# Performance work log

Hardware: AMD Instinct MI355X
Metric: run time of the kernel (lower is better)

## Reference

```python
import jax, jax.numpy as jnp
import numpy as np

N, E = 20000, 320000          # nodes, edges (avg degree 16)
IN, OUT, EC = 256, 256, 64    # in_channels == out_channels (required by BN placement)
BN_EPS = 1e-5


def setup_inputs() -> dict:
    key = jax.random.key(0)
    ks = jax.random.split(key, 8)
    def lin(k, fan_in, fan_out):
        # kaiming-uniform-ish init like nn.Linear
        bound = 1.0 / np.sqrt(fan_in)
        return jax.random.uniform(k, (fan_in, fan_out), jnp.float32, -bound, bound)
    return {
        "x": jax.random.normal(ks[0], (N, IN), jnp.float32),
        "edge_index": jax.random.randint(ks[1], (2, E), 0, N),
        "edge_attr": jax.random.normal(ks[2], (E, EC), jnp.float32),
        "W_edge": lin(ks[3], EC, IN),          # edge_lin (no bias)
        "W_rel": lin(ks[4], IN, OUT),           # GraphConv lin_rel weight
        "b_rel": jnp.zeros((OUT,), jnp.float32),  # GraphConv lin_rel bias
        "W_root": lin(ks[5], IN, OUT),          # GraphConv lin_root (no bias)
        "gamma": jnp.ones((OUT,), jnp.float32),  # BN weight
        "beta": jnp.zeros((OUT,), jnp.float32),  # BN bias
        "W_res": lin(ks[6], IN, OUT),           # res_lin (no bias)
    }


def reference(x, edge_index, edge_attr, W_edge, W_rel, b_rel, W_root, gamma, beta, W_res):
    src, dst = edge_index[0], edge_index[1]
    # edge feature projection: [E, EC] -> [E, IN]
    e = edge_attr @ W_edge
    # message passing: gather source node feats, modulate by edge feats, scatter-add to dst
    msg = x[src] * e                                   # [E, IN]
    agg = jax.ops.segment_sum(msg, dst, num_segments=x.shape[0])  # [N, IN]
    # GraphConv: lin_rel(aggregate) + lin_root(x)
    h = agg @ W_rel + b_rel + x @ W_root               # [N, OUT]
    h = jax.nn.relu(h)
    # BatchNorm1d (training mode: batch statistics over nodes)
    mean = h.mean(axis=0)
    var = ((h - mean) ** 2).mean(axis=0)
    h = (h - mean) * jax.lax.rsqrt(var + BN_EPS) * gamma + beta
    # residual branch
    return h + x @ W_res
```

## Files before the change

### kernel.cpp

```cpp
#include <hip/hip_runtime.h>
#include <hip/hip_bf16.h>


#define N_NODES 20000
#define E_EDGES 320000
#define C 256
#define CE 64
#define MAXDEG 64
#define BN_EPS 1e-5f

typedef __attribute__((ext_vector_type(8))) short short8;
typedef __attribute__((ext_vector_type(8))) unsigned short ushort8;
typedef __attribute__((ext_vector_type(4))) float f32x4;
typedef __attribute__((ext_vector_type(4))) unsigned short ushort4v;

static __device__ __forceinline__ float bf2f(unsigned short u) {
    union { unsigned int i; float f; } v; v.i = (unsigned int)u << 16; return v.f;
}
static __device__ __forceinline__ unsigned short f2bf(float f) {
    __hip_bfloat16 h = __float2bfloat16(f);
    return *reinterpret_cast<unsigned short*>(&h);
}

__global__ __launch_bounds__(256) void k_wprep(
    const float* __restrict__ W_rel, const float* __restrict__ W_root,
    const float* __restrict__ W_res, const float* __restrict__ W_edge,
    unsigned short* __restrict__ wt_hi, unsigned short* __restrict__ wte_hi) {
    int b = blockIdx.x, n = threadIdx.x;
    if (b < 768) {
        int m = b >> 8, k = b & 255;
        const float* W = (m == 0) ? W_rel : (m == 1) ? W_root : W_res;
        size_t o = (((size_t)m * 16 + (n >> 4)) * 8 + (k >> 5)) * 512
                 + (size_t)(((n & 15) | (((k >> 3) & 3) << 4)) * 8) + (k & 7);
        wt_hi[o] = f2bf(W[k * C + n]);
    } else {
        int k = b - 768;
        size_t o = ((size_t)(n >> 4) * 2 + (k >> 5)) * 512
                 + (size_t)(((n & 15) | (((k >> 3) & 3) << 4)) * 8) + (k & 7);
        wte_hi[o] = f2bf(W_edge[k * C + n]);
    }
}

__global__ void k_bucket(const int* __restrict__ ei, int* __restrict__ deg,
                         int2* __restrict__ elist2) {
    int e = blockIdx.x * blockDim.x + threadIdx.x;
    if (e < E_EDGES) {
        int d = ei[E_EDGES + e];
        int s = ei[e];
        int slot = atomicAdd(&deg[d], 1);
        if (slot < MAXDEG) elist2[d * MAXDEG + slot] = make_int2(e, s);
    }
}

__global__ __launch_bounds__(256, 3) void k_edgemm(
    const float* __restrict__ ea, const unsigned short* __restrict__ wte_hi,
    unsigned short* __restrict__ e_mat) {
    __shared__ short lds[16384];
    const int tid = threadIdx.x;
    const int e0 = blockIdx.x * 64;

#pragma unroll
    for (int i = 0; i < 4; ++i) {
        int f = tid + 256 * i;
        int r = f >> 4, k4 = (f & 15) * 4;
        float4 v = *reinterpret_cast<const float4*>(&ea[(size_t)(e0 + r) * CE + k4]);
        unsigned short h0 = f2bf(v.x), h1 = f2bf(v.y), h2 = f2bf(v.z), h3 = f2bf(v.w);
        ushort4v hv = {h0, h1, h2, h3};
        ushort4v lv = {f2bf(v.x - bf2f(h0)), f2bf(v.y - bf2f(h1)),
                       f2bf(v.z - bf2f(h2)), f2bf(v.w - bf2f(h3))};
        int rt = r >> 4, ks = k4 >> 5;
        int lane = (r & 15) | (((k4 >> 3) & 3) << 4);
        int base = (((rt * 2 + ks) * 2 + 0) * 64 + lane) * 8 + (k4 & 7);
        *reinterpret_cast<ushort4v*>(&lds[base]) = hv;
        *reinterpret_cast<ushort4v*>(&lds[base + 512]) = lv;
    }
    __syncthreads();

    const int w = tid >> 6, l = tid & 63;
    f32x4 acc[4][4];
#pragma unroll
    for (int rt = 0; rt < 4; ++rt)
#pragma unroll
        for (int ct = 0; ct < 4; ++ct) acc[rt][ct] = (f32x4){0.f, 0.f, 0.f, 0.f};

#pragma unroll
    for (int ks = 0; ks < 2; ++ks) {
        short8 b[4];
#pragma unroll
        for (int ct = 0; ct < 4; ++ct) {
            int nt = w * 4 + ct;
            b[ct] = *reinterpret_cast<const short8*>(&wte_hi[(size_t)(nt * 2 + ks) * 512 + l * 8]);
        }
        short8 ah[4], al[4];
#pragma unroll
        for (int rt = 0; rt < 4; ++rt) {
            int base = ((rt * 2 + ks) * 2) * 512 + l * 8;
            ah[rt] = *reinterpret_cast<const short8*>(&lds[base]);
            al[rt] = *reinterpret_cast<const short8*>(&lds[base + 512]);
        }
#pragma unroll
        for (int ct = 0; ct < 4; ++ct)
#pragma unroll
            for (int rt = 0; rt < 4; ++rt) {
                acc[rt][ct] = __builtin_amdgcn_mfma_f32_16x16x32_bf16(ah[rt], b[ct], acc[rt][ct], 0, 0, 0);
                acc[rt][ct] = __builtin_amdgcn_mfma_f32_16x16x32_bf16(al[rt], b[ct], acc[rt][ct], 0, 0, 0);
            }
    }

    __syncthreads();
#pragma unroll
    for (int rt = 0; rt < 4; ++rt)
#pragma unroll
        for (int ct = 0; ct < 4; ++ct) {
            int col = w * 64 + ct * 16 + (l & 15);
#pragma unroll
            for (int q = 0; q < 4; ++q) {
                int r = rt * 16 + (l >> 4) * 4 + q;
                lds[r * C + col] = (short)f2bf(acc[rt][ct][q]);
            }
        }
    __syncthreads();
#pragma unroll
    for (int i = 0; i < 8; ++i) {
        int f = tid + 256 * i;
        int r = f >> 5, c8 = (f & 31) * 8;
        *reinterpret_cast<ushort8*>(&e_mat[(size_t)(e0 + r) * C + c8]) =
            *reinterpret_cast<const ushort8*>(&lds[r * C + c8]);
    }
}

__global__ __launch_bounds__(128) void k_aggregate(
    const float* __restrict__ x, const unsigned short* __restrict__ e_mat,
    const int* __restrict__ deg, const int2* __restrict__ elist2,
    float* __restrict__ agg) {
    const int c2 = threadIdx.x;
    const int lane = threadIdx.x & 63;
    for (int node = blockIdx.x; node < N_NODES; node += gridDim.x) {
        int dr = deg[node];
        int d = __builtin_amdgcn_readfirstlane(dr < MAXDEG ? dr : MAXDEG);
        float accx = 0.f, accy = 0.f;
        if (d > 0) {
            int2 pr = elist2[node * MAXDEG + (lane < d ? lane : 0)];
            for (int i = 0; i < d; i += 4) {
                int m = d - i;
                unsigned int ev[4]; float2 xv[4];
#pragma unroll
                for (int j = 0; j < 4; ++j) {
                    if (j < m) {
                        int e = __shfl(pr.x, i + j);
                        int s = __shfl(pr.y, i + j);
                        ev[j] = *reinterpret_cast<const unsigned int*>(
                                    &e_mat[(size_t)e * C + c2 * 2]);
                        xv[j] = *reinterpret_cast<const float2*>(
                                    &x[(size_t)s * C + c2 * 2]);
                    } else { ev[j] = 0; xv[j] = make_float2(0.f, 0.f); }
                }
#pragma unroll
                for (int j = 0; j < 4; ++j) {
                    accx += bf2f((unsigned short)(ev[j] & 0xffff)) * xv[j].x;
                    accy += bf2f((unsigned short)(ev[j] >> 16)) * xv[j].y;
                }
            }
        }
        *reinterpret_cast<float2*>(&agg[(size_t)node * C + c2 * 2]) =
            make_float2(accx, accy);
    }
}

__global__ __launch_bounds__(256, 4) void k_gemm(
    const float* __restrict__ aggt, const float* __restrict__ x,
    const unsigned short* __restrict__ wt_hi,
    float* __restrict__ g_rel, float* __restrict__ g_root,
    float* __restrict__ g_res) {
    __shared__ short AB[16384];
    const int tid = threadIdx.x;
    const int n0 = blockIdx.x * 32;
    const int mat = blockIdx.y;
    const float* Asrc = (mat == 0) ? aggt : x;
    float* dst = (mat == 0) ? g_rel : (mat == 1) ? g_root : g_res;

#pragma unroll
    for (int i = 0; i < 8; ++i) {
        int f = tid + 256 * i;
        int r = f >> 6, k4 = (f & 63) * 4;
        float4 v = *reinterpret_cast<const float4*>(&Asrc[(size_t)(n0 + r) * C + k4]);
        unsigned short h0 = f2bf(v.x), h1 = f2bf(v.y), h2 = f2bf(v.z), h3 = f2bf(v.w);
        ushort4v hv = {h0, h1, h2, h3};
        ushort4v lv = {f2bf(v.x - bf2f(h0)), f2bf(v.y - bf2f(h1)),
                       f2bf(v.z - bf2f(h2)), f2bf(v.w - bf2f(h3))};
        int rt = r >> 4, ks = k4 >> 5;
        int lane = (r & 15) | (((k4 >> 3) & 3) << 4);
        int base = (((rt * 8 + ks) * 2 + 0) * 64 + lane) * 8 + (k4 & 7);
        *reinterpret_cast<ushort4v*>(&AB[base]) = hv;
        *reinterpret_cast<ushort4v*>(&AB[base + 512]) = lv;
    }
    __syncthreads();

    const int w = tid >> 6, l = tid & 63;
    f32x4 acc[2][4];
#pragma unroll
    for (int rt = 0; rt < 2; ++rt)
#pragma unroll
        for (int ct = 0; ct < 4; ++ct) acc[rt][ct] = (f32x4){0.f, 0.f, 0.f, 0.f};

    const unsigned short* wbase = wt_hi + (size_t)mat * 16 * 8 * 512;

#pragma unroll
    for (int ks = 0; ks < 8; ++ks) {
        short8 b[4];
#pragma unroll
        for (int ct = 0; ct < 4; ++ct) {
            int nt = w * 4 + ct;
            b[ct] = *reinterpret_cast<const short8*>(&wbase[(size_t)(nt * 8 + ks) * 512 + l * 8]);
        }
        short8 ah[2], al[2];
#pragma unroll
        for (int rt = 0; rt < 2; ++rt) {
            int base = ((rt * 8 + ks) * 2) * 512 + l * 8;
            ah[rt] = *reinterpret_cast<const short8*>(&AB[base]);
            al[rt] = *reinterpret_cast<const short8*>(&AB[base + 512]);
        }
#pragma unroll
        for (int ct = 0; ct < 4; ++ct)
#pragma unroll
            for (int rt = 0; rt < 2; ++rt) {
                acc[rt][ct] = __builtin_amdgcn_mfma_f32_16x16x32_bf16(ah[rt], b[ct], acc[rt][ct], 0, 0, 0);
                acc[rt][ct] = __builtin_amdgcn_mfma_f32_16x16x32_bf16(al[rt], b[ct], acc[rt][ct], 0, 0, 0);
            }
    }

#pragma unroll
    for (int ct = 0; ct < 4; ++ct) {
        int col = w * 64 + ct * 16 + (l & 15);
#pragma unroll
        for (int rt = 0; rt < 2; ++rt)
#pragma unroll
            for (int q = 0; q < 4; ++q) {
                int node = n0 + rt * 16 + (l >> 4) * 4 + q;
                dst[(size_t)node * C + col] = acc[rt][ct][q];
            }
    }
}

__global__ __launch_bounds__(256) void k_bnstat(
    const float* __restrict__ g_rel, const float* __restrict__ g_root,
    const float* __restrict__ b_rel, float* __restrict__ chsum,
    float* __restrict__ chsumsq) {
    __shared__ float2 red[4 * 256];
    const int tid = threadIdx.x;
    const int c0 = (tid & 63) * 4, rg = tid >> 6;
    const int base = blockIdx.x * 32;
    float4 b4 = *reinterpret_cast<const float4*>(&b_rel[c0]);
    float4 s1 = {0.f, 0.f, 0.f, 0.f}, s2 = {0.f, 0.f, 0.f, 0.f};
#pragma unroll
    for (int i = 0; i < 8; ++i) {
        size_t row = (size_t)(base + rg * 8 + i) * C + c0;
        float4 hr = *reinterpret_cast<const float4*>(&g_rel[row]);
        float4 ho = *reinterpret_cast<const float4*>(&g_root[row]);
        float4 h;
        h.x = fmaxf(hr.x + ho.x + b4.x, 0.f);
        h.y = fmaxf(hr.y + ho.y + b4.y, 0.f);
        h.z = fmaxf(hr.z + ho.z + b4.z, 0.f);
        h.w = fmaxf(hr.w + ho.w + b4.w, 0.f);
        s1.x += h.x; s1.y += h.y; s1.z += h.z; s1.w += h.w;
        s2.x += h.x * h.x; s2.y += h.y * h.y;
        s2.z += h.z * h.z; s2.w += h.w * h.w;
    }
    red[rg * 256 + c0 + 0] = make_float2(s1.x, s2.x);
    red[rg * 256 + c0 + 1] = make_float2(s1.y, s2.y);
    red[rg * 256 + c0 + 2] = make_float2(s1.z, s2.z);
    red[rg * 256 + c0 + 3] = make_float2(s1.w, s2.w);
    __syncthreads();
    float a = 0.f, bsum = 0.f;
#pragma unroll
    for (int g = 0; g < 4; ++g) {
        float2 v = red[g * 256 + tid];
        a += v.x; bsum += v.y;
    }
    atomicAdd(&chsum[tid], a);
    atomicAdd(&chsumsq[tid], bsum);
}

__global__ __launch_bounds__(256) void k_finalize(
    const float* __restrict__ g_rel, const float* __restrict__ g_root,
    const float* __restrict__ b_rel, const float* __restrict__ chsum,
    const float* __restrict__ chsumsq, const float* __restrict__ gamma,
    const float* __restrict__ beta, float* out) {
    const float invN = 1.f / (float)N_NODES;
    int i = (blockIdx.x * blockDim.x + threadIdx.x) * 4;
    if (i >= N_NODES * C) return;
    int c = i & (C - 1);
    float4 hr = *reinterpret_cast<const float4*>(&g_rel[i]);
    float4 ho = *reinterpret_cast<const float4*>(&g_root[i]);
    float4 b4 = *reinterpret_cast<const float4*>(&b_rel[c]);
    float4 rv = *reinterpret_cast<const float4*>(&out[i]);
    float4 o;
    {
        float h = fmaxf(hr.x + ho.x + b4.x, 0.f);
        float m = chsum[c + 0] * invN;
        float v = chsumsq[c + 0] * invN - m * m;
        o.x = (h - m) * rsqrtf(v + BN_EPS) * gamma[c + 0] + beta[c + 0] + rv.x;
    }
    {
        float h = fmaxf(hr.y + ho.y + b4.y, 0.f);
        float m = chsum[c + 1] * invN;
        float v = chsumsq[c + 1] * invN - m * m;
        o.y = (h - m) * rsqrtf(v + BN_EPS) * gamma[c + 1] + beta[c + 1] + rv.y;
    }
    {
        float h = fmaxf(hr.z + ho.z + b4.z, 0.f);
        float m = chsum[c + 2] * invN;
        float v = chsumsq[c + 2] * invN - m * m;
        o.z = (h - m) * rsqrtf(v + BN_EPS) * gamma[c + 2] + beta[c + 2] + rv.z;
    }
    {
        float h = fmaxf(hr.w + ho.w + b4.w, 0.f);
        float m = chsum[c + 3] * invN;
        float v = chsumsq[c + 3] * invN - m * m;
        o.w = (h - m) * rsqrtf(v + BN_EPS) * gamma[c + 3] + beta[c + 3] + rv.w;
    }
    *reinterpret_cast<float4*>(&out[i]) = o;
}

extern "C" void kernel_launch(void* const* d_in, const int* in_sizes, int n_in,
                              void* d_out, int out_size, void* d_ws, size_t ws_size,
                              hipStream_t stream) {
    const float* x      = (const float*)d_in[0];
    const int*   ei     = (const int*)  d_in[1];
    const float* ea     = (const float*)d_in[2];
    const float* W_edge = (const float*)d_in[3];
    const float* W_rel  = (const float*)d_in[4];
    const float* b_rel  = (const float*)d_in[5];
    const float* W_root = (const float*)d_in[6];
    const float* gamma  = (const float*)d_in[7];
    const float* beta   = (const float*)d_in[8];
    const float* W_res  = (const float*)d_in[9];
    float* out = (float*)d_out;

    float* ws      = (float*)d_ws;
    float* aggt    = ws;
    float* chsum   = ws + (size_t)N_NODES * C;
    float* chsumsq = chsum + C;
    int*   deg     = (int*)(chsumsq + C);
    int2*  elist2  = (int2*)(deg + N_NODES);
    unsigned short* e_mat  = (unsigned short*)(elist2 + (size_t)N_NODES * MAXDEG);
    unsigned short* wte_hi = e_mat + (size_t)E_EDGES * C;
    unsigned short* wt_hi  = wte_hi + C * CE;
    float* g_rel  = (float*)e_mat;
    float* g_root = g_rel + (size_t)N_NODES * C;
    size_t need = (char*)(wt_hi + 3 * C * C) - (char*)d_ws;
    if (ws_size < need) return;

    hipMemsetAsync(chsum, 0, 2 * C * sizeof(float) + N_NODES * sizeof(int), stream);

    k_wprep<<<832, 256, 0, stream>>>(W_rel, W_root, W_res, W_edge, wt_hi, wte_hi);
    k_bucket<<<(E_EDGES + 255) / 256, 256, 0, stream>>>(ei, deg, elist2);
    k_edgemm<<<E_EDGES / 64, 256, 0, stream>>>(ea, wte_hi, e_mat);
    k_aggregate<<<10000, 128, 0, stream>>>(x, e_mat, deg, elist2, aggt);
    k_gemm<<<dim3(N_NODES / 32, 3), 256, 0, stream>>>(aggt, x, wt_hi,
                                                      g_rel, g_root, out);
    k_bnstat<<<N_NODES / 32, 256, 0, stream>>>(g_rel, g_root, b_rel, chsum, chsumsq);
    k_finalize<<<(N_NODES * C / 4 + 255) / 256, 256, 0, stream>>>(
        g_rel, g_root, b_rel, chsum, chsumsq, gamma, beta, out);
}
```

Baseline: 335.9 us.

## Fuse edge projection GEMM into per-node aggregation kernel

Replaces the separate edge-feature GEMM (which wrote a bf16 E×256 edge matrix) and the aggregation kernel with one kernel per destination node. Each block gathers its incoming edges' attributes, projects them with MFMA into shared memory, then multiplies by gathered source features and sums. This removes the write and re-read of the large intermediate edge matrix. In exchange, edge_attr rows are gathered randomly, MFMA tiles are padded to multiples of 16 for low-degree nodes, and the kernel runs one block per node.

```diff
diff --git a/kernel.cpp b/kernel.cpp
--- a/kernel.cpp
+++ b/kernel.cpp
@@ -52,36 +52,58 @@
     }
 }
 
-__global__ __launch_bounds__(256, 3) void k_edgemm(
-    const float* __restrict__ ea, const unsigned short* __restrict__ wte_hi,
-    unsigned short* __restrict__ e_mat) {
+__global__ __launch_bounds__(256, 4) void k_fusedagg(
+    const float* __restrict__ x, const float* __restrict__ ea,
+    const unsigned short* __restrict__ wte_hi,
+    const int* __restrict__ deg, const int2* __restrict__ elist2,
+    float* __restrict__ agg) {
     __shared__ short lds[16384];
+    __shared__ int es[MAXDEG], ss[MAXDEG];
     const int tid = threadIdx.x;
-    const int e0 = blockIdx.x * 64;
+    const int node = blockIdx.x;
+
+    int dr = deg[node];
+    const int d = dr < MAXDEG ? dr : MAXDEG;
+    if (d == 0) {
+        agg[(size_t)node * C + tid] = 0.f;
+        return;
+    }
+    if (tid < d) {
+        int2 p = elist2[node * MAXDEG + tid];
+        es[tid] = p.x; ss[tid] = p.y;
+    }
+    __syncthreads();
+
+    const int rtmax = (d + 15) >> 4;
 
 #pragma unroll
     for (int i = 0; i < 4; ++i) {
         int f = tid + 256 * i;
         int r = f >> 4, k4 = (f & 15) * 4;
-        float4 v = *reinterpret_cast<const float4*>(&ea[(size_t)(e0 + r) * CE + k4]);
-        unsigned short h0 = f2bf(v.x), h1 = f2bf(v.y), h2 = f2bf(v.z), h3 = f2bf(v.w);
-        ushort4v hv = {h0, h1, h2, h3};
-        ushort4v lv = {f2bf(v.x - bf2f(h0)), f2bf(v.y - bf2f(h1)),
-                       f2bf(v.z - bf2f(h2)), f2bf(v.w - bf2f(h3))};
-        int rt = r >> 4, ks = k4 >> 5;
-        int lane = (r & 15) | (((k4 >> 3) & 3) << 4);
-        int base = (((rt * 2 + ks) * 2 + 0) * 64 + lane) * 8 + (k4 & 7);
-        *reinterpret_cast<ushort4v*>(&lds[base]) = hv;
-        *reinterpret_cast<ushort4v*>(&lds[base + 512]) = lv;
+        if (r < rtmax * 16) {
+            float4 v = {0.f, 0.f, 0.f, 0.f};
+            if (r < d)
+                v = *reinterpret_cast<const float4*>(&ea[(size_t)es[r] * CE + k4]);
+            unsigned short h0 = f2bf(v.x), h1 = f2bf(v.y), h2 = f2bf(v.z), h3 = f2bf(v.w);
+            ushort4v hv = {h0, h1, h2, h3};
+            ushort4v lv = {f2bf(v.x - bf2f(h0)), f2bf(v.y - bf2f(h1)),
+                           f2bf(v.z - bf2f(h2)), f2bf(v.w - bf2f(h3))};
+            int rt = r >> 4, ks = k4 >> 5;
+            int lane = (r & 15) | (((k4 >> 3) & 3) << 4);
+            int base = (((rt * 2 + ks) * 2 + 0) * 64 + lane) * 8 + (k4 & 7);
+            *reinterpret_cast<ushort4v*>(&lds[base]) = hv;
+            *reinterpret_cast<ushort4v*>(&lds[base + 512]) = lv;
+        }
     }
     __syncthreads();
 
     const int w = tid >> 6, l = tid & 63;
-    f32x4 acc[4][4];
-#pragma unroll
-    for (int rt = 0; rt < 4; ++rt)
+    f32x4 acc[2][4];
+#pragma unroll
+    for (int rt = 0; rt < 2; ++rt)
 #pragma unroll
         for (int ct = 0; ct < 4; ++ct) acc[rt][ct] = (f32x4){0.f, 0.f, 0.f, 0.f};
+    const int rtc = rtmax < 2 ? rtmax : 2;
 
 #pragma unroll
     for (int ks = 0; ks < 2; ++ks) {
@@ -91,25 +113,48 @@
             int nt = w * 4 + ct;
             b[ct] = *reinterpret_cast<const short8*>(&wte_hi[(size_t)(nt * 2 + ks) * 512 + l * 8]);
         }
-        short8 ah[4], al[4];
-#pragma unroll
-        for (int rt = 0; rt < 4; ++rt) {
+        for (int rt = 0; rt < rtc; ++rt) {
             int base = ((rt * 2 + ks) * 2) * 512 + l * 8;
-            ah[rt] = *reinterpret_cast<const short8*>(&lds[base]);
-            al[rt] = *reinterpret_cast<const short8*>(&lds[base + 512]);
-        }
-#pragma unroll
-        for (int ct = 0; ct < 4; ++ct)
-#pragma unroll
-            for (int rt = 0; rt < 4; ++rt) {
-                acc[rt][ct] = __builtin_amdgcn_mfma_f32_16x16x32_bf16(ah[rt], b[ct], acc[rt][ct], 0, 0, 0);
-                acc[rt][ct] = __builtin_amdgcn_mfma_f32_16x16x32_bf16(al[rt], b[ct], acc[rt][ct], 0, 0, 0);
-            }
-    }
-
-    __syncthreads();
-#pragma unroll
-    for (int rt = 0; rt < 4; ++rt)
+            short8 ah = *reinterpret_cast<const short8*>(&lds[base]);
+            short8 al = *reinterpret_cast<const short8*>(&lds[base + 512]);
+#pragma unroll
+            for (int ct = 0; ct < 4; ++ct) {
+                acc[rt][ct] = __builtin_amdgcn_mfma_f32_16x16x32_bf16(ah, b[ct], acc[rt][ct], 0, 0, 0);
+                acc[rt][ct] = __builtin_amdgcn_mfma_f32_16x16x32_bf16(al, b[ct], acc[rt][ct], 0, 0, 0);
+            }
+        }
+    }
+
+    f32x4 acc3[2][4];
+    const bool deep = (rtmax > 2);
+    if (deep) {
+#pragma unroll
+        for (int rt = 0; rt < 2; ++rt)
+#pragma unroll
+            for (int ct = 0; ct < 4; ++ct) acc3[rt][ct] = (f32x4){0.f, 0.f, 0.f, 0.f};
+#pragma unroll
+        for (int ks = 0; ks < 2; ++ks) {
+            short8 b[4];
+#pragma unroll
+            for (int ct = 0; ct < 4; ++ct) {
+                int nt = w * 4 + ct;
+                b[ct] = *reinterpret_cast<const short8*>(&wte_hi[(size_t)(nt * 2 + ks) * 512 + l * 8]);
+            }
+            for (int rt = 2; rt < rtmax; ++rt) {
+                int base = ((rt * 2 + ks) * 2) * 512 + l * 8;
+                short8 ah = *reinterpret_cast<const short8*>(&lds[base]);
+                short8 al = *reinterpret_cast<const short8*>(&lds[base + 512]);
+#pragma unroll
+                for (int ct = 0; ct < 4; ++ct) {
+                    acc3[rt - 2][ct] = __builtin_amdgcn_mfma_f32_16x16x32_bf16(ah, b[ct], acc3[rt - 2][ct], 0, 0, 0);
+                    acc3[rt - 2][ct] = __builtin_amdgcn_mfma_f32_16x16x32_bf16(al, b[ct], acc3[rt - 2][ct], 0, 0, 0);
+                }
+            }
+        }
+    }
+
+    __syncthreads();
+    for (int rt = 0; rt < rtc; ++rt)
 #pragma unroll
         for (int ct = 0; ct < 4; ++ct) {
             int col = w * 64 + ct * 16 + (l & 15);
@@ -119,52 +164,36 @@
                 lds[r * C + col] = (short)f2bf(acc[rt][ct][q]);
             }
         }
-    __syncthreads();
-#pragma unroll
-    for (int i = 0; i < 8; ++i) {
-        int f = tid + 256 * i;
-        int r = f >> 5, c8 = (f & 31) * 8;
-        *reinterpret_cast<ushort8*>(&e_mat[(size_t)(e0 + r) * C + c8]) =
-            *reinterpret_cast<const ushort8*>(&lds[r * C + c8]);
-    }
-}
-
-__global__ __launch_bounds__(128) void k_aggregate(
-    const float* __restrict__ x, const unsigned short* __restrict__ e_mat,
-    const int* __restrict__ deg, const int2* __restrict__ elist2,
-    float* __restrict__ agg) {
-    const int c2 = threadIdx.x;
-    const int lane = threadIdx.x & 63;
-    for (int node = blockIdx.x; node < N_NODES; node += gridDim.x) {
-        int dr = deg[node];
-        int d = __builtin_amdgcn_readfirstlane(dr < MAXDEG ? dr : MAXDEG);
-        float accx = 0.f, accy = 0.f;
-        if (d > 0) {
-            int2 pr = elist2[node * MAXDEG + (lane < d ? lane : 0)];
-            for (int i = 0; i < d; i += 4) {
-                int m = d - i;
-                unsigned int ev[4]; float2 xv[4];
-#pragma unroll
-                for (int j = 0; j < 4; ++j) {
-                    if (j < m) {
-                        int e = __shfl(pr.x, i + j);
-                        int s = __shfl(pr.y, i + j);
-                        ev[j] = *reinterpret_cast<const unsigned int*>(
-                                    &e_mat[(size_t)e * C + c2 * 2]);
-                        xv[j] = *reinterpret_cast<const float2*>(
-                                    &x[(size_t)s * C + c2 * 2]);
-                    } else { ev[j] = 0; xv[j] = make_float2(0.f, 0.f); }
+    if (deep) {
+        for (int rt = 2; rt < rtmax; ++rt)
+#pragma unroll
+            for (int ct = 0; ct < 4; ++ct) {
+                int col = w * 64 + ct * 16 + (l & 15);
+#pragma unroll
+                for (int q = 0; q < 4; ++q) {
+                    int r = rt * 16 + (l >> 4) * 4 + q;
+                    lds[r * C + col] = (short)f2bf(acc3[rt - 2][ct][q]);
                 }
-#pragma unroll
-                for (int j = 0; j < 4; ++j) {
-                    accx += bf2f((unsigned short)(ev[j] & 0xffff)) * xv[j].x;
-                    accy += bf2f((unsigned short)(ev[j] >> 16)) * xv[j].y;
-                }
-            }
-        }
-        *reinterpret_cast<float2*>(&agg[(size_t)node * C + c2 * 2]) =
-            make_float2(accx, accy);
-    }
+            }
+    }
+    __syncthreads();
+
+    const int c = tid;
+    float accv = 0.f;
+    for (int i = 0; i < d; i += 4) {
+        int m = d - i;
+        float xv[4], ev[4];
+#pragma unroll
+        for (int j = 0; j < 4; ++j) {
+            if (j < m) {
+                xv[j] = x[(size_t)ss[i + j] * C + c];
+                ev[j] = bf2f((unsigned short)lds[(i + j) * C + c]);
+            } else { xv[j] = 0.f; ev[j] = 0.f; }
+        }
+#pragma unroll
+        for (int j = 0; j < 4; ++j) accv += ev[j] * xv[j];
+    }
+    agg[(size_t)node * C + c] = accv;
 }
 
 __global__ __launch_bounds__(256, 4) void k_gemm(
@@ -343,11 +372,10 @@
     float* chsumsq = chsum + C;
     int*   deg     = (int*)(chsumsq + C);
     int2*  elist2  = (int2*)(deg + N_NODES);
-    unsigned short* e_mat  = (unsigned short*)(elist2 + (size_t)N_NODES * MAXDEG);
-    unsigned short* wte_hi = e_mat + (size_t)E_EDGES * C;
+    float* g_rel   = (float*)(elist2 + (size_t)N_NODES * MAXDEG);
+    float* g_root  = g_rel + (size_t)N_NODES * C;
+    unsigned short* wte_hi = (unsigned short*)(g_root + (size_t)N_NODES * C);
     unsigned short* wt_hi  = wte_hi + C * CE;
-    float* g_rel  = (float*)e_mat;
-    float* g_root = g_rel + (size_t)N_NODES * C;
     size_t need = (char*)(wt_hi + 3 * C * C) - (char*)d_ws;
     if (ws_size < need) return;
 
@@ -355,8 +383,7 @@
 
     k_wprep<<<832, 256, 0, stream>>>(W_rel, W_root, W_res, W_edge, wt_hi, wte_hi);
     k_bucket<<<(E_EDGES + 255) / 256, 256, 0, stream>>>(ei, deg, elist2);
-    k_edgemm<<<E_EDGES / 64, 256, 0, stream>>>(ea, wte_hi, e_mat);
-    k_aggregate<<<10000, 128, 0, stream>>>(x, e_mat, deg, elist2, aggt);
+    k_fusedagg<<<N_NODES, 256, 0, stream>>>(x, ea, wte_hi, deg, elist2, aggt);
     k_gemm<<<dim3(N_NODES / 32, 3), 256, 0, stream>>>(aggt, x, wt_hi,
                                                       g_rel, g_root, out);
     k_bnstat<<<N_NODES / 32, 256, 0, stream>>>(g_rel, g_root, b_rel, chsum, chsumsq);
```

Result: slower. 354.3 us (+5.5%).
